# Kernel optimization log

Hardware: AMD Instinct MI355X
Metric: run time of the kernel (lower is better)

The kernel has to match this reference:

```python
import math
import jax, jax.numpy as jnp
import numpy as np

B, H, HKV, T, D = 2, 32, 8, 2048, 128
NEG = -1e9  # additive causal-mask value (matches HF large-negative masking)


def setup_inputs() -> dict:
    key = jax.random.key(0)
    k1, k2, k3 = jax.random.split(key, 3)
    query = jax.random.normal(k1, (B, H, T, D), dtype=jnp.float32)
    k = jax.random.normal(k2, (B, HKV, T, D), dtype=jnp.float32)
    v = jax.random.normal(k3, (B, HKV, T, D), dtype=jnp.float32)
    scale_attn = jnp.asarray(math.sqrt(D), dtype=jnp.float32)
    # causal additive mask [B, 1, T, T]: 0 on/below diagonal, NEG above
    causal = jnp.tril(jnp.ones((T, T), dtype=bool))
    attention_mask = jnp.where(causal, 0.0, NEG).astype(jnp.float32)
    attention_mask = jnp.broadcast_to(attention_mask[None, None], (B, 1, T, T))
    return {"query": query, "key": k, "value": v,
            "scale_attn": scale_attn, "attention_mask": attention_mask}


def reference(query, key, value, scale_attn, attention_mask):
    # GQA: repeat kv heads to match query heads (repeat_interleave on head axis)
    n_rep = query.shape[1] // key.shape[1]
    k = jnp.repeat(key, n_rep, axis=1)    # [B,H,S,D]
    v = jnp.repeat(value, n_rep, axis=1)  # [B,H,S,D]
    # QK^T / scale + mask
    attn_weights = jnp.einsum("bhtd,bhsd->bhts", query, k) / scale_attn
    attn_weights = attn_weights + attention_mask
    # softmax in fp32, cast back to query dtype (matches torch ref)
    attn_weights = jax.nn.softmax(attn_weights.astype(jnp.float32), axis=-1)
    attn_weights = attn_weights.astype(query.dtype)
    attn_output = jnp.einsum("bhts,bhsd->bhtd", attn_weights, v)
    return attn_output
```

## Files before the change

kernel.cpp:

```cpp
#include <hip/hip_runtime.h>
#include <hip/hip_bf16.h>

namespace {

constexpr int Bb = 2, Hh = 32, HKVc = 8, Tt = 2048, Dd = 128;
constexpr int BQ = 128, BKV = 32, NW = 8, NQB = Tt / BQ;
constexpr int KLD = 136;
constexpr int VLD = 40;
constexpr int PLD = 40;
constexpr float LOG2E = 1.44269504088896340736f;
constexpr float MSC = 8.0f * LOG2E;

typedef float  f32x4  __attribute__((ext_vector_type(4)));
typedef short  bf16x8 __attribute__((ext_vector_type(8)));
typedef unsigned int u32;
typedef u32    u32x2  __attribute__((ext_vector_type(2)));

__device__ inline u32 cvtpk(float a, float b) {
  u32 r;
  asm("v_cvt_pk_bf16_f32 %0, %1, %2" : "=v"(r) : "v"(a), "v"(b));
  return r;
}

__global__ __launch_bounds__(512, 4) void fattn_kernel(const float* __restrict__ Q,
                                                       const float* __restrict__ K,
                                                       const float* __restrict__ V,
                                                       const float* __restrict__ scale_p,
                                                       float* __restrict__ O) {
  __shared__ short Klds[2][BKV * KLD];
  __shared__ short Vt[2][Dd * VLD];
  __shared__ short Plds[NW * 16 * PLD];

  const int pp = blockIdx.x >> 6;
  const int bh = blockIdx.x & 63;
  const int b = bh >> 5, h = bh & 31, hkv = h >> 2;

  const int tid = threadIdx.x;
  const int w = tid >> 6, lane = tid & 63, l15 = lane & 15, g = lane >> 4;
  const float qsc = LOG2E / scale_p[0];

  const float* kbase = K + (size_t)(b * HKVc + hkv) * Tt * Dd;
  const float* vbase = V + (size_t)(b * HKVc + hkv) * Tt * Dd;

  const int krow = tid >> 5, kc4 = tid & 31;
  const int vc = tid & 31, kv0 = 2 * (tid >> 5);

  short* Pw = Plds + w * 16 * PLD;

  bf16x8 ones;
#pragma unroll
  for (int i = 0; i < 8; ++i) ones[i] = (short)0x3F80;

#pragma unroll 1
  for (int seg = 0; seg < 2; ++seg) {
    const int qb = (seg == 0) ? (NQB - 1 - pp) : pp;
    const int qrow0 = qb * BQ + w * 16;
    const int nt = 4 * qb + 4;

    bf16x8 qf[4];
    {
      const float* qp = Q + ((size_t)(b * Hh + h) * Tt + qrow0 + l15) * Dd;
#pragma unroll
      for (int kk = 0; kk < 4; ++kk) {
        f32x4 a = *(const f32x4*)(qp + kk * 32 + g * 8);
        f32x4 c = *(const f32x4*)(qp + kk * 32 + g * 8 + 4);
        u32* qd = (u32*)&qf[kk];
        qd[0] = cvtpk(a[0] * qsc, a[1] * qsc);
        qd[1] = cvtpk(a[2] * qsc, a[3] * qsc);
        qd[2] = cvtpk(c[0] * qsc, c[1] * qsc);
        qd[3] = cvtpk(c[2] * qsc, c[3] * qsc);
      }
    }

    f32x4 acc[8];
#pragma unroll
    for (int n = 0; n < 8; ++n) { acc[n][0] = 0.f; acc[n][1] = 0.f; acc[n][2] = 0.f; acc[n][3] = 0.f; }
    f32x4 accl;
    accl[0] = 0.f; accl[1] = 0.f; accl[2] = 0.f; accl[3] = 0.f;

    {
      f32x4 k0 = *(const f32x4*)(kbase + (size_t)krow * Dd + kc4 * 4);
      f32x4 k1 = *(const f32x4*)(kbase + (size_t)(krow + 16) * Dd + kc4 * 4);
      float vr[8];
#pragma unroll
      for (int j = 0; j < 4; ++j) {
        vr[2 * j]     = vbase[(size_t)kv0 * Dd + vc + 32 * j];
        vr[2 * j + 1] = vbase[(size_t)(kv0 + 1) * Dd + vc + 32 * j];
      }
      u32x2 kp;
      kp[0] = cvtpk(k0[0], k0[1]); kp[1] = cvtpk(k0[2], k0[3]);
      *(u32x2*)&Klds[0][krow * KLD + kc4 * 4] = kp;
      kp[0] = cvtpk(k1[0], k1[1]); kp[1] = cvtpk(k1[2], k1[3]);
      *(u32x2*)&Klds[0][(krow + 16) * KLD + kc4 * 4] = kp;
#pragma unroll
      for (int j = 0; j < 4; ++j)
        *(u32*)&Vt[0][(vc + 32 * j) * VLD + kv0] = cvtpk(vr[2 * j], vr[2 * j + 1]);
    }
    __syncthreads();

    for (int t = 0; t < nt; ++t) {
      const int cur = t & 1, nxt = cur ^ 1;
      const bool more = (t + 1 < nt);
      f32x4 kr0, kr1;
      float vr[8];
      if (more) {
        const float* ks = kbase + (size_t)(t + 1) * BKV * Dd;
        const float* vs = vbase + (size_t)(t + 1) * BKV * Dd;
        kr0 = *(const f32x4*)(ks + (size_t)krow * Dd + kc4 * 4);
        kr1 = *(const f32x4*)(ks + (size_t)(krow + 16) * Dd + kc4 * 4);
#pragma unroll
        for (int j = 0; j < 4; ++j) {
          vr[2 * j]     = vs[(size_t)kv0 * Dd + vc + 32 * j];
          vr[2 * j + 1] = vs[(size_t)(kv0 + 1) * Dd + vc + 32 * j];
        }
      }

      const int col0 = t * BKV;
      if (col0 <= qrow0 + 15) {
        f32x4 s0{}, s1{};
#pragma unroll
        for (int kk = 0; kk < 4; ++kk) {
          bf16x8 k0 = *(const bf16x8*)&Klds[cur][l15 * KLD + kk * 32 + g * 8];
          bf16x8 k1 = *(const bf16x8*)&Klds[cur][(16 + l15) * KLD + kk * 32 + g * 8];
          s0 = __builtin_amdgcn_mfma_f32_16x16x32_bf16(qf[kk], k0, s0, 0, 0, 0);
          s1 = __builtin_amdgcn_mfma_f32_16x16x32_bf16(qf[kk], k1, s1, 0, 0, 0);
        }

        const bool needm = (col0 + 31 > qrow0);
#pragma unroll
        for (int r = 0; r < 4; ++r) {
          const int qr = qrow0 + 4 * g + r;
          float p0 = exp2f(s0[r] - MSC);
          float p1 = exp2f(s1[r] - MSC);
          if (needm) {
            if (col0 + l15 > qr)      p0 = 0.f;
            if (col0 + 16 + l15 > qr) p1 = 0.f;
          }
          u32 pk = cvtpk(p0, p1);
          Pw[(4 * g + r) * PLD + l15]      = (short)(pk & 0xffffu);
          Pw[(4 * g + r) * PLD + 16 + l15] = (short)(pk >> 16);
        }

        bf16x8 pa = *(const bf16x8*)&Pw[l15 * PLD + g * 8];
        accl = __builtin_amdgcn_mfma_f32_16x16x32_bf16(pa, ones, accl, 0, 0, 0);
#pragma unroll
        for (int n = 0; n < 8; ++n) {
          bf16x8 vf = *(const bf16x8*)&Vt[cur][(n * 16 + l15) * VLD + g * 8];
          acc[n] = __builtin_amdgcn_mfma_f32_16x16x32_bf16(pa, vf, acc[n], 0, 0, 0);
        }
      }

      if (more) {
        u32x2 kp;
        kp[0] = cvtpk(kr0[0], kr0[1]); kp[1] = cvtpk(kr0[2], kr0[3]);
        *(u32x2*)&Klds[nxt][krow * KLD + kc4 * 4] = kp;
        kp[0] = cvtpk(kr1[0], kr1[1]); kp[1] = cvtpk(kr1[2], kr1[3]);
        *(u32x2*)&Klds[nxt][(krow + 16) * KLD + kc4 * 4] = kp;
#pragma unroll
        for (int j = 0; j < 4; ++j)
          *(u32*)&Vt[nxt][(vc + 32 * j) * VLD + kv0] = cvtpk(vr[2 * j], vr[2 * j + 1]);
      }
      __syncthreads();
    }

    float* op = O + ((size_t)(b * Hh + h) * Tt + qrow0) * Dd;
#pragma unroll
    for (int r = 0; r < 4; ++r) {
      float inv_l = 1.0f / accl[r];
#pragma unroll
      for (int n = 0; n < 8; ++n) {
        op[(size_t)(4 * g + r) * Dd + n * 16 + l15] = acc[n][r] * inv_l;
      }
    }
  }
}

}

extern "C" void kernel_launch(void* const* d_in, const int* in_sizes, int n_in,
                              void* d_out, int out_size, void* d_ws, size_t ws_size,
                              hipStream_t stream) {
  const float* Q = (const float*)d_in[0];
  const float* K = (const float*)d_in[1];
  const float* V = (const float*)d_in[2];
  const float* s = (const float*)d_in[3];
  float* O = (float*)d_out;
  dim3 grid((NQB / 2) * Bb * Hh);
  fattn_kernel<<<grid, NW * 64, 0, stream>>>(Q, K, V, s, O);
}
```

Baseline: 139.4 us.

## Pre-convert K/V to swizzled bf16 tiles and use 32x32 MFMA main kernel

Adds a prep kernel that converts K and V once per KV head into bf16 tiles in the workspace, with V pre-transposed and both XOR-swizzled. The main kernel streams these tiles straight into LDS with global_load_lds, so the fp32 loads and conversions are no longer repeated for every query block and GQA head. It also switches to 32x32x16 MFMA with 32 query rows per wave, 4 waves per block, one query block per workgroup, and computes the row sums in registers with shuffles instead of a ones-matrix MFMA. The cost is an extra launch and workspace traffic, plus a less balanced causal grid, with the old kernel kept as a fallback when the workspace is too small.

```diff
diff --git a/kernel.cpp b/kernel.cpp
--- a/kernel.cpp
+++ b/kernel.cpp
@@ -4,17 +4,15 @@
 namespace {
 
 constexpr int Bb = 2, Hh = 32, HKVc = 8, Tt = 2048, Dd = 128;
-constexpr int BQ = 128, BKV = 32, NW = 8, NQB = Tt / BQ;
-constexpr int KLD = 136;
-constexpr int VLD = 40;
-constexpr int PLD = 40;
 constexpr float LOG2E = 1.44269504088896340736f;
 constexpr float MSC = 8.0f * LOG2E;
 
 typedef float  f32x4  __attribute__((ext_vector_type(4)));
+typedef float  f32x16 __attribute__((ext_vector_type(16)));
 typedef short  bf16x8 __attribute__((ext_vector_type(8)));
 typedef unsigned int u32;
 typedef u32    u32x2  __attribute__((ext_vector_type(2)));
+typedef u32    u32x4  __attribute__((ext_vector_type(4)));
 
 __device__ inline u32 cvtpk(float a, float b) {
   u32 r;
@@ -22,41 +20,208 @@
   return r;
 }
 
-__global__ __launch_bounds__(512, 4) void fattn_kernel(const float* __restrict__ Q,
-                                                       const float* __restrict__ K,
-                                                       const float* __restrict__ V,
-                                                       const float* __restrict__ scale_p,
-                                                       float* __restrict__ O) {
-  __shared__ short Klds[2][BKV * KLD];
-  __shared__ short Vt[2][Dd * VLD];
-  __shared__ short Plds[NW * 16 * PLD];
-
+__device__ inline void gload_lds16(const void* g, void* l) {
+  __builtin_amdgcn_global_load_lds((const __attribute__((address_space(1))) unsigned int*)g,
+                                   (__attribute__((address_space(3))) unsigned int*)l, 16, 0, 0);
+}
+
+__global__ __launch_bounds__(256) void prep_kernel(const float* __restrict__ K,
+                                                   const float* __restrict__ V,
+                                                   short* __restrict__ Kb, short* __restrict__ Vb) {
+  __shared__ float Vlds[32][132];
+  const int blk = blockIdx.x;
+  const int tid = threadIdx.x;
+  const float* ksrc = K + (size_t)blk * 32 * Dd;
+  const float* vsrc = V + (size_t)blk * 32 * Dd;
+  short* kdst = Kb + (size_t)blk * 4096;
+  short* vdst = Vb + (size_t)blk * 4096;
+
+#pragma unroll
+  for (int i = 0; i < 2; ++i) {
+    int idx = tid + i * 256;
+    int row = idx >> 4, c = idx & 15;
+    int d0 = 8 * (c ^ (row & 7));
+    f32x4 a = *(const f32x4*)(ksrc + row * Dd + d0);
+    f32x4 b = *(const f32x4*)(ksrc + row * Dd + d0 + 4);
+    u32x4 ov;
+    ov[0] = cvtpk(a[0], a[1]); ov[1] = cvtpk(a[2], a[3]);
+    ov[2] = cvtpk(b[0], b[1]); ov[3] = cvtpk(b[2], b[3]);
+    *(u32x4*)(kdst + (size_t)idx * 8) = ov;
+  }
+#pragma unroll
+  for (int i = 0; i < 4; ++i) {
+    int idx = tid + i * 256;
+    int row = idx >> 5, c4 = idx & 31;
+    *(f32x4*)&Vlds[row][c4 * 4] = *(const f32x4*)(vsrc + row * Dd + c4 * 4);
+  }
+  __syncthreads();
+#pragma unroll
+  for (int i = 0; i < 2; ++i) {
+    int idx = tid + i * 256;
+    int d = idx >> 2, c = idx & 3;
+    int kv0 = 8 * (c ^ ((d >> 1) & 3));
+    u32x4 ov;
+    ov[0] = cvtpk(Vlds[kv0 + 0][d], Vlds[kv0 + 1][d]);
+    ov[1] = cvtpk(Vlds[kv0 + 2][d], Vlds[kv0 + 3][d]);
+    ov[2] = cvtpk(Vlds[kv0 + 4][d], Vlds[kv0 + 5][d]);
+    ov[3] = cvtpk(Vlds[kv0 + 6][d], Vlds[kv0 + 7][d]);
+    *(u32x4*)(vdst + (size_t)idx * 8) = ov;
+  }
+}
+
+__global__ __launch_bounds__(256, 3) void fattn_main(const float* __restrict__ Q,
+                                                     const short* __restrict__ Kb,
+                                                     const short* __restrict__ Vb,
+                                                     const float* __restrict__ scale_p,
+                                                     float* __restrict__ O) {
+  __shared__ short Klds[2][4096];
+  __shared__ short Vt[2][4096];
+  __shared__ short Plds[4][32 * 40];
+
+  const int z = blockIdx.x;
+  const int qb = 15 - (z >> 6);
+  const int bh = z & 63;
+  const int b = bh >> 5, h = bh & 31, hkv = h >> 2;
+
+  const int tid = threadIdx.x;
+  const int w = tid >> 6, lane = tid & 63;
+  const int l31 = lane & 31, hh = lane >> 5;
+
+  const float qsc = LOG2E / scale_p[0];
+
+  const int qrow0 = qb * 128 + w * 32;
+  const int nt = 4 * qb + 4;
+
+  const short* ktiles = Kb + (size_t)(b * HKVc + hkv) * 64 * 4096;
+  const short* vtiles = Vb + (size_t)(b * HKVc + hkv) * 64 * 4096;
+
+  bf16x8 qf[8];
+  {
+    const float* qp = Q + ((size_t)(b * Hh + h) * Tt + qrow0 + l31) * Dd;
+#pragma unroll
+    for (int kk = 0; kk < 8; ++kk) {
+      const float* p0 = qp + kk * 16 + hh * 8;
+      f32x4 a = *(const f32x4*)(p0);
+      f32x4 c = *(const f32x4*)(p0 + 4);
+      u32* qd = (u32*)&qf[kk];
+      qd[0] = cvtpk(a[0] * qsc, a[1] * qsc);
+      qd[1] = cvtpk(a[2] * qsc, a[3] * qsc);
+      qd[2] = cvtpk(c[0] * qsc, c[1] * qsc);
+      qd[3] = cvtpk(c[2] * qsc, c[3] * qsc);
+    }
+  }
+
+  f32x16 acc[4];
+#pragma unroll
+  for (int n = 0; n < 4; ++n)
+#pragma unroll
+    for (int i = 0; i < 16; ++i) acc[n][i] = 0.f;
+  float lsum[16];
+#pragma unroll
+  for (int i = 0; i < 16; ++i) lsum[i] = 0.f;
+
+  short* Pw = &Plds[4 > 1 ? w : 0][0];
+
+#pragma unroll
+  for (int i = 0; i < 2; ++i) {
+    gload_lds16(ktiles + (size_t)(tid + i * 256) * 8, &Klds[0][(w * 64 + i * 256) * 8]);
+    gload_lds16(vtiles + (size_t)(tid + i * 256) * 8, &Vt[0][(w * 64 + i * 256) * 8]);
+  }
+  __syncthreads();
+
+  for (int t = 0; t < nt; ++t) {
+    const int cur = t & 1, nxt = cur ^ 1;
+    if (t + 1 < nt) {
+      const short* kt = ktiles + (size_t)(t + 1) * 4096;
+      const short* vt = vtiles + (size_t)(t + 1) * 4096;
+#pragma unroll
+      for (int i = 0; i < 2; ++i) {
+        gload_lds16(kt + (size_t)(tid + i * 256) * 8, &Klds[nxt][(w * 64 + i * 256) * 8]);
+        gload_lds16(vt + (size_t)(tid + i * 256) * 8, &Vt[nxt][(w * 64 + i * 256) * 8]);
+      }
+    }
+
+    const int col0 = t * 32;
+    if (col0 <= qrow0 + 31) {
+      f32x16 s;
+#pragma unroll
+      for (int i = 0; i < 16; ++i) s[i] = 0.f;
+#pragma unroll
+      for (int kk = 0; kk < 8; ++kk) {
+        bf16x8 kf = *(const bf16x8*)((const char*)&Klds[cur][0] + l31 * 256 +
+                                     ((((kk * 2 + hh)) ^ (l31 & 7)) << 4));
+        s = __builtin_amdgcn_mfma_f32_32x32x16_bf16(qf[kk], kf, s, 0, 0, 0);
+      }
+
+      const bool needm = (col0 + 31 > qrow0);
+#pragma unroll
+      for (int r = 0; r < 16; ++r) {
+        const int rowp = (r & 3) + 8 * (r >> 2) + 4 * hh;
+        float p = exp2f(s[r] - MSC);
+        if (needm && (col0 + l31 > qrow0 + rowp)) p = 0.f;
+        lsum[r] += p;
+        Pw[rowp * 40 + l31] = (short)cvtpk(p, p);
+      }
+
+#pragma unroll
+      for (int kf = 0; kf < 2; ++kf) {
+        bf16x8 pa = *(const bf16x8*)((const char*)Pw + l31 * 80 + kf * 32 + hh * 16);
+#pragma unroll
+        for (int n = 0; n < 4; ++n) {
+          const int dd = n * 32 + l31;
+          bf16x8 vf = *(const bf16x8*)((const char*)&Vt[cur][0] + dd * 64 +
+                                       (((kf * 2 + hh) ^ ((dd >> 1) & 3)) << 4));
+          acc[n] = __builtin_amdgcn_mfma_f32_32x32x16_bf16(pa, vf, acc[n], 0, 0, 0);
+        }
+      }
+    }
+    __syncthreads();
+  }
+
+#pragma unroll
+  for (int r = 0; r < 16; ++r) {
+    float v = lsum[r];
+    v += __shfl_xor(v, 1); v += __shfl_xor(v, 2); v += __shfl_xor(v, 4);
+    v += __shfl_xor(v, 8); v += __shfl_xor(v, 16);
+    lsum[r] = 1.0f / v;
+  }
+  float* op = O + ((size_t)(b * Hh + h) * Tt + qrow0) * Dd;
+#pragma unroll
+  for (int r = 0; r < 16; ++r) {
+    const int rowp = (r & 3) + 8 * (r >> 2) + 4 * hh;
+#pragma unroll
+    for (int n = 0; n < 4; ++n)
+      op[(size_t)rowp * Dd + n * 32 + l31] = acc[n][r] * lsum[r];
+  }
+}
+
+constexpr int FBKV = 32, FNW = 8, FNQB = 16;
+constexpr int FKLD = 136, FVLD = 40, FPLD = 40;
+
+__global__ __launch_bounds__(512, 4) void fattn_fb(const float* __restrict__ Q,
+                                                   const float* __restrict__ K,
+                                                   const float* __restrict__ V,
+                                                   const float* __restrict__ scale_p,
+                                                   float* __restrict__ O) {
+  __shared__ short Klds[2][FBKV * FKLD];
+  __shared__ short Vt[2][Dd * FVLD];
+  __shared__ short Plds[FNW * 16 * FPLD];
   const int pp = blockIdx.x >> 6;
   const int bh = blockIdx.x & 63;
   const int b = bh >> 5, h = bh & 31, hkv = h >> 2;
-
   const int tid = threadIdx.x;
   const int w = tid >> 6, lane = tid & 63, l15 = lane & 15, g = lane >> 4;
   const float qsc = LOG2E / scale_p[0];
-
   const float* kbase = K + (size_t)(b * HKVc + hkv) * Tt * Dd;
   const float* vbase = V + (size_t)(b * HKVc + hkv) * Tt * Dd;
-
   const int krow = tid >> 5, kc4 = tid & 31;
   const int vc = tid & 31, kv0 = 2 * (tid >> 5);
-
-  short* Pw = Plds + w * 16 * PLD;
-
-  bf16x8 ones;
-#pragma unroll
-  for (int i = 0; i < 8; ++i) ones[i] = (short)0x3F80;
-
+  short* Pw = Plds + w * 16 * FPLD;
 #pragma unroll 1
   for (int seg = 0; seg < 2; ++seg) {
-    const int qb = (seg == 0) ? (NQB - 1 - pp) : pp;
-    const int qrow0 = qb * BQ + w * 16;
+    const int qb = (seg == 0) ? (FNQB - 1 - pp) : pp;
+    const int qrow0 = qb * 128 + w * 16;
     const int nt = 4 * qb + 4;
-
     bf16x8 qf[4];
     {
       const float* qp = Q + ((size_t)(b * Hh + h) * Tt + qrow0 + l15) * Dd;
@@ -65,67 +230,61 @@
         f32x4 a = *(const f32x4*)(qp + kk * 32 + g * 8);
         f32x4 c = *(const f32x4*)(qp + kk * 32 + g * 8 + 4);
         u32* qd = (u32*)&qf[kk];
-        qd[0] = cvtpk(a[0] * qsc, a[1] * qsc);
-        qd[1] = cvtpk(a[2] * qsc, a[3] * qsc);
-        qd[2] = cvtpk(c[0] * qsc, c[1] * qsc);
-        qd[3] = cvtpk(c[2] * qsc, c[3] * qsc);
-      }
-    }
-
+        qd[0] = cvtpk(a[0] * qsc, a[1] * qsc); qd[1] = cvtpk(a[2] * qsc, a[3] * qsc);
+        qd[2] = cvtpk(c[0] * qsc, c[1] * qsc); qd[3] = cvtpk(c[2] * qsc, c[3] * qsc);
+      }
+    }
     f32x4 acc[8];
 #pragma unroll
-    for (int n = 0; n < 8; ++n) { acc[n][0] = 0.f; acc[n][1] = 0.f; acc[n][2] = 0.f; acc[n][3] = 0.f; }
-    f32x4 accl;
-    accl[0] = 0.f; accl[1] = 0.f; accl[2] = 0.f; accl[3] = 0.f;
-
+    for (int n = 0; n < 8; ++n) { acc[n][0]=0.f; acc[n][1]=0.f; acc[n][2]=0.f; acc[n][3]=0.f; }
+    f32x4 accl; accl[0]=0.f; accl[1]=0.f; accl[2]=0.f; accl[3]=0.f;
+    bf16x8 ones;
+#pragma unroll
+    for (int i = 0; i < 8; ++i) ones[i] = (short)0x3F80;
     {
       f32x4 k0 = *(const f32x4*)(kbase + (size_t)krow * Dd + kc4 * 4);
       f32x4 k1 = *(const f32x4*)(kbase + (size_t)(krow + 16) * Dd + kc4 * 4);
       float vr[8];
 #pragma unroll
       for (int j = 0; j < 4; ++j) {
-        vr[2 * j]     = vbase[(size_t)kv0 * Dd + vc + 32 * j];
-        vr[2 * j + 1] = vbase[(size_t)(kv0 + 1) * Dd + vc + 32 * j];
+        vr[2*j]   = vbase[(size_t)kv0 * Dd + vc + 32 * j];
+        vr[2*j+1] = vbase[(size_t)(kv0+1) * Dd + vc + 32 * j];
       }
       u32x2 kp;
       kp[0] = cvtpk(k0[0], k0[1]); kp[1] = cvtpk(k0[2], k0[3]);
-      *(u32x2*)&Klds[0][krow * KLD + kc4 * 4] = kp;
+      *(u32x2*)&Klds[0][krow * FKLD + kc4 * 4] = kp;
       kp[0] = cvtpk(k1[0], k1[1]); kp[1] = cvtpk(k1[2], k1[3]);
-      *(u32x2*)&Klds[0][(krow + 16) * KLD + kc4 * 4] = kp;
+      *(u32x2*)&Klds[0][(krow + 16) * FKLD + kc4 * 4] = kp;
 #pragma unroll
       for (int j = 0; j < 4; ++j)
-        *(u32*)&Vt[0][(vc + 32 * j) * VLD + kv0] = cvtpk(vr[2 * j], vr[2 * j + 1]);
+        *(u32*)&Vt[0][(vc + 32 * j) * FVLD + kv0] = cvtpk(vr[2*j], vr[2*j+1]);
     }
     __syncthreads();
-
     for (int t = 0; t < nt; ++t) {
       const int cur = t & 1, nxt = cur ^ 1;
       const bool more = (t + 1 < nt);
-      f32x4 kr0, kr1;
-      float vr[8];
+      f32x4 kr0, kr1; float vr[8];
       if (more) {
-        const float* ks = kbase + (size_t)(t + 1) * BKV * Dd;
-        const float* vs = vbase + (size_t)(t + 1) * BKV * Dd;
+        const float* ks = kbase + (size_t)(t + 1) * FBKV * Dd;
+        const float* vs = vbase + (size_t)(t + 1) * FBKV * Dd;
         kr0 = *(const f32x4*)(ks + (size_t)krow * Dd + kc4 * 4);
         kr1 = *(const f32x4*)(ks + (size_t)(krow + 16) * Dd + kc4 * 4);
 #pragma unroll
         for (int j = 0; j < 4; ++j) {
-          vr[2 * j]     = vs[(size_t)kv0 * Dd + vc + 32 * j];
-          vr[2 * j + 1] = vs[(size_t)(kv0 + 1) * Dd + vc + 32 * j];
-        }
-      }
-
-      const int col0 = t * BKV;
+          vr[2*j]   = vs[(size_t)kv0 * Dd + vc + 32 * j];
+          vr[2*j+1] = vs[(size_t)(kv0+1) * Dd + vc + 32 * j];
+        }
+      }
+      const int col0 = t * FBKV;
       if (col0 <= qrow0 + 15) {
         f32x4 s0{}, s1{};
 #pragma unroll
         for (int kk = 0; kk < 4; ++kk) {
-          bf16x8 k0 = *(const bf16x8*)&Klds[cur][l15 * KLD + kk * 32 + g * 8];
-          bf16x8 k1 = *(const bf16x8*)&Klds[cur][(16 + l15) * KLD + kk * 32 + g * 8];
+          bf16x8 k0 = *(const bf16x8*)&Klds[cur][l15 * FKLD + kk * 32 + g * 8];
+          bf16x8 k1 = *(const bf16x8*)&Klds[cur][(16 + l15) * FKLD + kk * 32 + g * 8];
           s0 = __builtin_amdgcn_mfma_f32_16x16x32_bf16(qf[kk], k0, s0, 0, 0, 0);
           s1 = __builtin_amdgcn_mfma_f32_16x16x32_bf16(qf[kk], k1, s1, 0, 0, 0);
         }
-
         const bool needm = (col0 + 31 > qrow0);
 #pragma unroll
         for (int r = 0; r < 4; ++r) {
@@ -137,41 +296,38 @@
             if (col0 + 16 + l15 > qr) p1 = 0.f;
           }
           u32 pk = cvtpk(p0, p1);
-          Pw[(4 * g + r) * PLD + l15]      = (short)(pk & 0xffffu);
-          Pw[(4 * g + r) * PLD + 16 + l15] = (short)(pk >> 16);
-        }
-
-        bf16x8 pa = *(const bf16x8*)&Pw[l15 * PLD + g * 8];
+          Pw[(4 * g + r) * FPLD + l15]      = (short)(pk & 0xffffu);
+          Pw[(4 * g + r) * FPLD + 16 + l15] = (short)(pk >> 16);
+        }
+        bf16x8 pa = *(const bf16x8*)&Pw[l15 * FPLD + g * 8];
         accl = __builtin_amdgcn_mfma_f32_16x16x32_bf16(pa, ones, accl, 0, 0, 0);
 #pragma unroll
         for (int n = 0; n < 8; ++n) {
-          bf16x8 vf = *(const bf16x8*)&Vt[cur][(n * 16 + l15) * VLD + g * 8];
+          bf16x8 vf = *(const bf16x8*)&Vt[cur][(n * 16 + l15) * FVLD + g * 8];
           acc[n] = __builtin_amdgcn_mfma_f32_16x16x32_bf16(pa, vf, acc[n], 0, 0, 0);
         }
       }
-
       if (more) {
         u32x2 kp;
         kp[0] = cvtpk(kr0[0], kr0[1]); kp[1] = cvtpk(kr0[2], kr0[3]);
-        *(u32x2*)&Klds[nxt][krow * KLD + kc4 * 4] = kp;
+        *(u32x2*)&Klds[nxt][krow * FKLD + kc4 * 4] = kp;
         kp[0] = cvtpk(kr1[0], kr1[1]); kp[1] = cvtpk(kr1[2], kr1[3]);
-        *(u32x2*)&Klds[nxt][(krow + 16) * KLD + kc4 * 4] = kp;
+        *(u32x2*)&Klds[nxt][(krow + 16) * FKLD + kc4 * 4] = kp;
 #pragma unroll
         for (int j = 0; j < 4; ++j)
-          *(u32*)&Vt[nxt][(vc + 32 * j) * VLD + kv0] = cvtpk(vr[2 * j], vr[2 * j + 1]);
+          *(u32*)&Vt[nxt][(vc + 32 * j) * FVLD + kv0] = cvtpk(vr[2*j], vr[2*j+1]);
       }
       __syncthreads();
     }
-
     float* op = O + ((size_t)(b * Hh + h) * Tt + qrow0) * Dd;
 #pragma unroll
     for (int r = 0; r < 4; ++r) {
       float inv_l = 1.0f / accl[r];
 #pragma unroll
-      for (int n = 0; n < 8; ++n) {
+      for (int n = 0; n < 8; ++n)
         op[(size_t)(4 * g + r) * Dd + n * 16 + l15] = acc[n][r] * inv_l;
-      }
-    }
+    }
+    __syncthreads();
   }
 }
 
@@ -185,6 +341,14 @@
   const float* V = (const float*)d_in[2];
   const float* s = (const float*)d_in[3];
   float* O = (float*)d_out;
-  dim3 grid((NQB / 2) * Bb * Hh);
-  fattn_kernel<<<grid, NW * 64, 0, stream>>>(Q, K, V, s, O);
-}
+  const size_t ntile = (size_t)Bb * HKVc * (Tt / 32);
+  const size_t need = 2 * ntile * 4096 * sizeof(short);
+  if (ws_size >= need) {
+    short* Kb = (short*)d_ws;
+    short* Vb = Kb + ntile * 4096;
+    prep_kernel<<<dim3((unsigned)ntile), 256, 0, stream>>>(K, V, Kb, Vb);
+    fattn_main<<<dim3(16 * Bb * Hh), 256, 0, stream>>>(Q, Kb, Vb, s, O);
+  } else {
+    fattn_fb<<<dim3(8 * Bb * Hh), 512, 0, stream>>>(Q, K, V, s, O);
+  }
+}
```

Measured after the change: 135.7 us. 1.03x faster.
